# Optimization experiments

Hardware: AMD Instinct MI355X
Metric: run time of the kernel (lower is better)

Reference implementation:

```python
import jax, jax.numpy as jnp
import numpy as np

H = 64  # hidden size
T = 11  # unrolled timesteps


def setup_inputs() -> dict:
    key = jax.random.key(0)
    ks = jax.random.split(key, 8)
    B, V, E = 65536, 50000, 100
    return {
        "sent": jax.random.randint(ks[0], (B, T), 0, V, dtype=jnp.int32),
        "emb_W": jax.random.normal(ks[1], (V, E), jnp.float32) * 0.05,
        "W_ih": jax.random.normal(ks[2], (4 * H, E), jnp.float32) * 0.05,
        "W_hh": jax.random.normal(ks[3], (4 * H, H), jnp.float32) * 0.05,
        "b_ih": jax.random.normal(ks[4], (4 * H,), jnp.float32) * 0.05,
        "b_hh": jax.random.normal(ks[5], (4 * H,), jnp.float32) * 0.05,
        "fc_W": jax.random.normal(ks[6], (14, H), jnp.float32) * 0.05,
        "fc_b": jax.random.normal(ks[7], (14,), jnp.float32) * 0.05,
    }


def _lstm_cell(x, h, c, W_ih, W_hh, b_ih, b_hh):
    # gates order in torch LSTMCell: i, f, g, o
    gates = x @ W_ih.T + b_ih + h @ W_hh.T + b_hh  # [B, 4H]
    i, f, g, o = jnp.split(gates, 4, axis=-1)
    c_new = jax.nn.sigmoid(f) * c + jax.nn.sigmoid(i) * jnp.tanh(g)
    h_new = jax.nn.sigmoid(o) * jnp.tanh(c_new)
    return h_new, c_new


def reference(sent, emb_W, W_ih, W_hh, b_ih, b_hh, fc_W, fc_b):
    embed = emb_W[sent]  # [B, T, E]
    B = embed.shape[0]
    h0 = jnp.zeros((B, H), embed.dtype)
    c0 = jnp.zeros((B, H), embed.dtype)
    xs = jnp.swapaxes(embed[:, :T, :], 0, 1)  # [T, B, E]

    def step(carry, x):
        h, c = carry
        h, c = _lstm_cell(x, h, c, W_ih, W_hh, b_ih, b_hh)
        return (h, c), None

    (h_last, _), _ = jax.lax.scan(step, (h0, c0), xs)
    logits = h_last @ fc_W.T + fc_b  # [B, 14]
    return jax.nn.log_softmax(logits, axis=-1)
```

## Files before the change

kernel.cpp:

```cpp
#include <hip/hip_runtime.h>
#include <hip/hip_bf16.h>

#define T_STEPS 11
#define E_DIM   100
#define XSL     2048
#define NDMA    (2 * T_STEPS)

typedef int   i32x4   __attribute__((ext_vector_type(4)));
typedef float f32x4   __attribute__((ext_vector_type(4)));
typedef _Float16 h16x2 __attribute__((ext_vector_type(2)));
typedef _Float16 h16x4 __attribute__((ext_vector_type(4)));
typedef _Float16 h16x8 __attribute__((ext_vector_type(8)));

typedef __attribute__((address_space(1))) const unsigned int g_as1;
typedef __attribute__((address_space(3))) unsigned int l_as3;

__device__ __forceinline__ h16x2 spl2(float v) {
    _Float16 h = (_Float16)v;
    return (h16x2){h, h};
}
__device__ __forceinline__ h16x2 pk2(float a, float b) {
    return __builtin_bit_cast(h16x2, __builtin_amdgcn_cvt_pkrtz(a, b));
}
__device__ __forceinline__ unsigned char f2fp8(float f) {
    return (unsigned char)(__builtin_amdgcn_cvt_pk_fp8_f32(f, 0.f, 0, false) & 0xff);
}
__device__ __forceinline__ long long ll_lo(i32x4 v) {
    return ((long long)(unsigned)v[1] << 32) | (unsigned)v[0];
}
__device__ __forceinline__ long long ll_hi(i32x4 v) {
    return ((long long)(unsigned)v[3] << 32) | (unsigned)v[2];
}

__device__ __forceinline__ h16x2 tanh5(h16x2 x) {
    h16x2 x2 = x * x;
    h16x2 p = x2 * spl2(0.13333333f) + spl2(-0.33333333f);
    p = x2 * p + spl2(1.0f);
    return x * p;
}
__device__ __forceinline__ h16x2 tanh7(h16x2 x) {
    h16x2 x2 = x * x;
    h16x2 p = x2 * spl2(-0.05396825f) + spl2(0.13333333f);
    p = x2 * p + spl2(-0.33333333f);
    p = x2 * p + spl2(1.0f);
    return x * p;
}
__device__ __forceinline__ h16x2 sig3(h16x2 x) {
    h16x2 x2 = x * x;
    h16x2 p = x2 * spl2(-0.020833334f) + spl2(0.25f);
    return x * p + spl2(0.5f);
}

__global__ void pack_all(const float* __restrict__ emb,
                         const float* __restrict__ W_ih, const float* __restrict__ W_hh,
                         const float* __restrict__ b_ih, const float* __restrict__ b_hh,
                         unsigned char* __restrict__ embp8, unsigned char* __restrict__ Wx8,
                         unsigned char* __restrict__ Wh8, float* __restrict__ biasf, int V)
{
    int b = blockIdx.x;
    int tid = threadIdx.x;
    if (b < 128) {
        int id = b * 256 + tid;
        int n = id >> 7, k = id & 127;
        float v = (k < E_DIM) ? W_ih[n * E_DIM + k] : 0.f;
        int kt = k >> 5;
        int lane = (n & 15) | (((k & 31) >> 3) << 4);
        Wx8[((kt * 16 + (n >> 4)) * 64 + lane) * 8 + (k & 7)] = f2fp8(v);
    } else if (b < 192) {
        int id = (b - 128) * 256 + tid;
        int n = id >> 6, k = id & 63;
        int kt = k >> 5;
        int lane = (n & 15) | (((k & 31) >> 3) << 4);
        Wh8[((kt * 16 + (n >> 4)) * 64 + lane) * 8 + (k & 7)] = f2fp8(W_hh[n * 64 + k]);
    } else if (b == 192) {
        biasf[tid] = b_ih[tid] + b_hh[tid];
    } else {
        int id = (b - 193) * 256 + tid;
        if (id >= V * 8) return;
        int row = id >> 3;
        int c8 = id & 7;
        int p = c8 >> 2, qq = c8 & 3;
        const float* xr = emb + (size_t)row * E_DIM;
        float v[16];
        #pragma unroll
        for (int w = 0; w < 16; ++w) {
            int k = p * 64 + (w >> 3) * 32 + qq * 8 + (w & 7);
            v[w] = (k < E_DIM) ? xr[k] : 0.f;
        }
        int4 o;
        int* op = &o.x;
        #pragma unroll
        for (int w = 0; w < 4; ++w) {
            int d = __builtin_amdgcn_cvt_pk_fp8_f32(v[w*4+0], v[w*4+1], 0, false);
            d = __builtin_amdgcn_cvt_pk_fp8_f32(v[w*4+2], v[w*4+3], d, true);
            op[w] = d;
        }
        *reinterpret_cast<int4*>(embp8 + (size_t)row * 128 + c8 * 16) = o;
    }
}

template<int PACKED>
__global__ __launch_bounds__(256, 4)
void lstm_fused(const int* __restrict__ sent,
                const float* __restrict__ emb, const unsigned char* __restrict__ embp8,
                const unsigned char* __restrict__ Wx8, const unsigned char* __restrict__ Wh8,
                const float* __restrict__ biasf,
                const float* __restrict__ fc_W, const float* __restrict__ fc_b,
                float* __restrict__ out)
{
    __shared__ unsigned char xlds[T_STEPS * XSL];
    __shared__ unsigned char hlds[2][1024];
    __shared__ float biaslds[256];
    __shared__ short hscr[16 * 68];
    const int tid  = threadIdx.x;
    const int wv   = tid >> 6;
    const int lane = tid & 63;
    const int r    = lane & 15;
    const int q    = lane >> 4;
    const int b0   = blockIdx.x * 16;

    for (int d = wv; d < NDMA; d += 4) {
        int sl = d >> 1, half = d & 1;
        int c  = half * 4 + (lane >> 4);
        int rr = lane & 15;
        int idx = sent[(b0 + rr) * T_STEPS + sl];
        if (PACKED) {
            const unsigned char* src = embp8 + (size_t)idx * 128 + c * 16;
            __builtin_amdgcn_global_load_lds(
                (g_as1*)src, (l_as3*)&xlds[sl * XSL + half * 1024], 16, 0, 0);
        } else {
            const float* xr = emb + (size_t)idx * E_DIM;
            int p = c >> 2, qq = c & 3;
            float v[16];
            #pragma unroll
            for (int w = 0; w < 16; ++w) {
                int k = p * 64 + (w >> 3) * 32 + qq * 8 + (w & 7);
                v[w] = (k < E_DIM) ? xr[k] : 0.f;
            }
            int4 o;
            int* op = &o.x;
            #pragma unroll
            for (int w = 0; w < 4; ++w) {
                int dd = __builtin_amdgcn_cvt_pk_fp8_f32(v[w*4+0], v[w*4+1], 0, false);
                dd = __builtin_amdgcn_cvt_pk_fp8_f32(v[w*4+2], v[w*4+3], dd, true);
                op[w] = dd;
            }
            *reinterpret_cast<int4*>(&xlds[sl * XSL + (half * 64 + lane) * 16]) = o;
        }
    }

    long long wx[4][4], wh[2][4];
    #pragma unroll
    for (int kt = 0; kt < 4; ++kt)
        #pragma unroll
        for (int g = 0; g < 4; ++g)
            wx[kt][g] = *reinterpret_cast<const long long*>(
                Wx8 + ((kt * 16 + g * 4 + wv) * 64 + lane) * 8);
    #pragma unroll
    for (int kt = 0; kt < 2; ++kt)
        #pragma unroll
        for (int g = 0; g < 4; ++g)
            wh[kt][g] = *reinterpret_cast<const long long*>(
                Wh8 + ((kt * 16 + g * 4 + wv) * 64 + lane) * 8);
    #pragma unroll
    for (int kt = 0; kt < 4; ++kt)
        #pragma unroll
        for (int g = 0; g < 4; ++g)
            asm volatile("" : "+v"(wx[kt][g]));
    #pragma unroll
    for (int kt = 0; kt < 2; ++kt)
        #pragma unroll
        for (int g = 0; g < 4; ++g)
            asm volatile("" : "+v"(wh[kt][g]));

    biaslds[tid] = biasf[tid];
    reinterpret_cast<int*>(&hlds[0][0])[tid] = 0;

    __builtin_amdgcn_s_waitcnt(0);
    __syncthreads();

    auto acc_bias_x = [&](int sl, f32x4* acc) {
        #pragma unroll
        for (int g = 0; g < 4; ++g)
            acc[g] = *reinterpret_cast<const f32x4*>(
                &biaslds[(g * 4 + wv) * 16 + q * 4]);
        #pragma unroll
        for (int p = 0; p < 2; ++p) {
            i32x4 v = *reinterpret_cast<const i32x4*>(
                &xlds[sl * XSL + ((p * 4 + q) * 16 + r) * 16]);
            long long lo = ll_lo(v), hi = ll_hi(v);
            #pragma unroll
            for (int g = 0; g < 4; ++g)
                acc[g] = __builtin_amdgcn_mfma_f32_16x16x32_fp8_fp8(wx[2*p][g], lo, acc[g], 0, 0, 0);
            #pragma unroll
            for (int g = 0; g < 4; ++g)
                acc[g] = __builtin_amdgcn_mfma_f32_16x16x32_fp8_fp8(wx[2*p+1][g], hi, acc[g], 0, 0, 0);
        }
    };

    h16x2 c01 = spl2(0.f), c23 = spl2(0.f);
    f32x4 acc[4];
    acc_bias_x(0, acc);

    const int hq  = (wv & 1) * 2 + (q >> 1);
    const int hoff = (hq * 16 + r) * 16 + (wv >> 1) * 8 + (q & 1) * 4;

    #pragma unroll
    for (int t = 0; t < T_STEPS; ++t) {
        i32x4 hv = *reinterpret_cast<const i32x4*>(&hlds[t & 1][(q * 16 + r) * 16]);
        long long bh0 = ll_lo(hv), bh1 = ll_hi(hv);
        #pragma unroll
        for (int g = 0; g < 4; ++g)
            acc[g] = __builtin_amdgcn_mfma_f32_16x16x32_fp8_fp8(wh[0][g], bh0, acc[g], 0, 0, 0);
        #pragma unroll
        for (int g = 0; g < 4; ++g)
            acc[g] = __builtin_amdgcn_mfma_f32_16x16x32_fp8_fp8(wh[1][g], bh1, acc[g], 0, 0, 0);

        h16x2 gi0 = pk2(acc[0][0], acc[0][1]), gi1 = pk2(acc[0][2], acc[0][3]);
        h16x2 gf0 = pk2(acc[1][0], acc[1][1]), gf1 = pk2(acc[1][2], acc[1][3]);
        h16x2 gg0 = pk2(acc[2][0], acc[2][1]), gg1 = pk2(acc[2][2], acc[2][3]);
        h16x2 go0 = pk2(acc[3][0], acc[3][1]), go1 = pk2(acc[3][2], acc[3][3]);
        c01 = sig3(gf0) * c01 + sig3(gi0) * tanh5(gg0);
        c23 = sig3(gf1) * c23 + sig3(gi1) * tanh5(gg1);
        h16x2 h01 = sig3(go0) * tanh7(c01);
        h16x2 h23 = sig3(go1) * tanh7(c23);

        int hw = __builtin_amdgcn_cvt_pk_fp8_f32((float)h01[0], (float)h01[1], 0, false);
        hw = __builtin_amdgcn_cvt_pk_fp8_f32((float)h23[0], (float)h23[1], hw, true);
        *reinterpret_cast<int*>(&hlds[(t + 1) & 1][hoff]) = hw;

        if (t == T_STEPS - 1) {
            h16x4 hn = { h01[0], h01[1], h23[0], h23[1] };
            *reinterpret_cast<h16x4*>(&hscr[r * 68 + wv * 16 + q * 4]) = hn;
        }

        if (t + 1 < T_STEPS) acc_bias_x(t + 1, acc);

        __syncthreads();
    }

    const int row_local = wv * 4 + q;
    const int cls = r;
    const int brow = b0 + row_local;
    float s = (cls < 14) ? fc_b[cls] : 0.f;
    const float* wrow = fc_W + ((cls < 14) ? cls : 0) * 64;
    #pragma unroll
    for (int ch = 0; ch < 8; ++ch) {
        h16x8 hv8 = *reinterpret_cast<const h16x8*>(&hscr[row_local * 68 + ch * 8]);
        #pragma unroll
        for (int j = 0; j < 8; ++j)
            s = fmaf((float)hv8[j], wrow[ch * 8 + j], s);
    }
    float lg = (cls < 14) ? s : -1e30f;
    float mx = lg;
    mx = fmaxf(mx, __shfl_xor(mx, 1));
    mx = fmaxf(mx, __shfl_xor(mx, 2));
    mx = fmaxf(mx, __shfl_xor(mx, 4));
    mx = fmaxf(mx, __shfl_xor(mx, 8));
    float se = __expf(lg - mx);
    se += __shfl_xor(se, 1);
    se += __shfl_xor(se, 2);
    se += __shfl_xor(se, 4);
    se += __shfl_xor(se, 8);
    float lse = mx + __logf(se);
    if (cls < 14) out[(size_t)brow * 14 + cls] = lg - lse;
}

extern "C" void kernel_launch(void* const* d_in, const int* in_sizes, int n_in,
                              void* d_out, int out_size, void* d_ws, size_t ws_size,
                              hipStream_t stream)
{
    const int*   sent = (const int*)d_in[0];
    const float* emb  = (const float*)d_in[1];
    const float* W_ih = (const float*)d_in[2];
    const float* W_hh = (const float*)d_in[3];
    const float* b_ih = (const float*)d_in[4];
    const float* b_hh = (const float*)d_in[5];
    const float* fc_W = (const float*)d_in[6];
    const float* fc_b = (const float*)d_in[7];
    float* out = (float*)d_out;

    const int B = in_sizes[0] / T_STEPS;
    const int V = in_sizes[1] / E_DIM;
    const size_t emb_bytes = (size_t)V * 128;
    const size_t need = emb_bytes + 32768 + 16384 + 1024;
    const bool packed = ws_size >= need;

    unsigned char* embp8 = (unsigned char*)d_ws;
    unsigned char* Wx8   = embp8 + emb_bytes;
    unsigned char* Wh8   = Wx8 + 32768;
    float*         biasf = (float*)(Wh8 + 16384);
    if (!packed) {
        Wx8   = (unsigned char*)d_ws;
        Wh8   = Wx8 + 32768;
        biasf = (float*)(Wh8 + 16384);
        embp8 = nullptr;
    }

    const int grid = B / 16;
    if (packed) {
        int pgrid = 193 + (V * 8 + 255) / 256;
        pack_all<<<pgrid, 256, 0, stream>>>(emb, W_ih, W_hh, b_ih, b_hh,
                                            embp8, Wx8, Wh8, biasf, V);
        lstm_fused<1><<<grid, 256, 0, stream>>>(sent, emb, embp8, Wx8, Wh8,
                                                biasf, fc_W, fc_b, out);
    } else {
        pack_all<<<193, 256, 0, stream>>>(emb, W_ih, W_hh, b_ih, b_hh,
                                          nullptr, Wx8, Wh8, biasf, 0);
        lstm_fused<0><<<grid, 256, 0, stream>>>(sent, emb, nullptr, Wx8, Wh8,
                                                biasf, fc_W, fc_b, out);
    }
}
```

Baseline: 150.5 us.

## Gather fp32 embedding rows directly and drop the fp8 embedding pre-pack pass

```diff
diff --git a/kernel.cpp b/kernel.cpp
--- a/kernel.cpp
+++ b/kernel.cpp
@@ -4,7 +4,7 @@
 #define T_STEPS 11
 #define E_DIM   100
 #define XSL     2048
-#define NDMA    (2 * T_STEPS)
+#define NSTG    (2 * T_STEPS)
 
 typedef int   i32x4   __attribute__((ext_vector_type(4)));
 typedef float f32x4   __attribute__((ext_vector_type(4)));
@@ -12,9 +12,6 @@
 typedef _Float16 h16x4 __attribute__((ext_vector_type(4)));
 typedef _Float16 h16x8 __attribute__((ext_vector_type(8)));
 
-typedef __attribute__((address_space(1))) const unsigned int g_as1;
-typedef __attribute__((address_space(3))) unsigned int l_as3;
-
 __device__ __forceinline__ h16x2 spl2(float v) {
     _Float16 h = (_Float16)v;
     return (h16x2){h, h};
@@ -24,6 +21,10 @@
 }
 __device__ __forceinline__ unsigned char f2fp8(float f) {
     return (unsigned char)(__builtin_amdgcn_cvt_pk_fp8_f32(f, 0.f, 0, false) & 0xff);
+}
+__device__ __forceinline__ int pk8x4(f32x4 v) {
+    int d = __builtin_amdgcn_cvt_pk_fp8_f32(v[0], v[1], 0, false);
+    return __builtin_amdgcn_cvt_pk_fp8_f32(v[2], v[3], d, true);
 }
 __device__ __forceinline__ long long ll_lo(i32x4 v) {
     return ((long long)(unsigned)v[1] << 32) | (unsigned)v[0];
@@ -51,11 +52,10 @@
     return x * p + spl2(0.5f);
 }
 
-__global__ void pack_all(const float* __restrict__ emb,
-                         const float* __restrict__ W_ih, const float* __restrict__ W_hh,
+__global__ void pack_all(const float* __restrict__ W_ih, const float* __restrict__ W_hh,
                          const float* __restrict__ b_ih, const float* __restrict__ b_hh,
-                         unsigned char* __restrict__ embp8, unsigned char* __restrict__ Wx8,
-                         unsigned char* __restrict__ Wh8, float* __restrict__ biasf, int V)
+                         unsigned char* __restrict__ Wx8, unsigned char* __restrict__ Wh8,
+                         float* __restrict__ biasf)
 {
     int b = blockIdx.x;
     int tid = threadIdx.x;
@@ -72,37 +72,14 @@
         int kt = k >> 5;
         int lane = (n & 15) | (((k & 31) >> 3) << 4);
         Wh8[((kt * 16 + (n >> 4)) * 64 + lane) * 8 + (k & 7)] = f2fp8(W_hh[n * 64 + k]);
-    } else if (b == 192) {
+    } else {
         biasf[tid] = b_ih[tid] + b_hh[tid];
-    } else {
-        int id = (b - 193) * 256 + tid;
-        if (id >= V * 8) return;
-        int row = id >> 3;
-        int c8 = id & 7;
-        int p = c8 >> 2, qq = c8 & 3;
-        const float* xr = emb + (size_t)row * E_DIM;
-        float v[16];
-        #pragma unroll
-        for (int w = 0; w < 16; ++w) {
-            int k = p * 64 + (w >> 3) * 32 + qq * 8 + (w & 7);
-            v[w] = (k < E_DIM) ? xr[k] : 0.f;
-        }
-        int4 o;
-        int* op = &o.x;
-        #pragma unroll
-        for (int w = 0; w < 4; ++w) {
-            int d = __builtin_amdgcn_cvt_pk_fp8_f32(v[w*4+0], v[w*4+1], 0, false);
-            d = __builtin_amdgcn_cvt_pk_fp8_f32(v[w*4+2], v[w*4+3], d, true);
-            op[w] = d;
-        }
-        *reinterpret_cast<int4*>(embp8 + (size_t)row * 128 + c8 * 16) = o;
-    }
-}
-
-template<int PACKED>
+    }
+}
+
 __global__ __launch_bounds__(256, 4)
 void lstm_fused(const int* __restrict__ sent,
-                const float* __restrict__ emb, const unsigned char* __restrict__ embp8,
+                const float* __restrict__ emb,
                 const unsigned char* __restrict__ Wx8, const unsigned char* __restrict__ Wh8,
                 const float* __restrict__ biasf,
                 const float* __restrict__ fc_W, const float* __restrict__ fc_b,
@@ -119,34 +96,26 @@
     const int q    = lane >> 4;
     const int b0   = blockIdx.x * 16;
 
-    for (int d = wv; d < NDMA; d += 4) {
+    for (int d = wv; d < NSTG; d += 4) {
         int sl = d >> 1, half = d & 1;
         int c  = half * 4 + (lane >> 4);
         int rr = lane & 15;
         int idx = sent[(b0 + rr) * T_STEPS + sl];
-        if (PACKED) {
-            const unsigned char* src = embp8 + (size_t)idx * 128 + c * 16;
-            __builtin_amdgcn_global_load_lds(
-                (g_as1*)src, (l_as3*)&xlds[sl * XSL + half * 1024], 16, 0, 0);
-        } else {
-            const float* xr = emb + (size_t)idx * E_DIM;
-            int p = c >> 2, qq = c & 3;
-            float v[16];
-            #pragma unroll
-            for (int w = 0; w < 16; ++w) {
-                int k = p * 64 + (w >> 3) * 32 + qq * 8 + (w & 7);
-                v[w] = (k < E_DIM) ? xr[k] : 0.f;
-            }
-            int4 o;
-            int* op = &o.x;
-            #pragma unroll
-            for (int w = 0; w < 4; ++w) {
-                int dd = __builtin_amdgcn_cvt_pk_fp8_f32(v[w*4+0], v[w*4+1], 0, false);
-                dd = __builtin_amdgcn_cvt_pk_fp8_f32(v[w*4+2], v[w*4+3], dd, true);
-                op[w] = dd;
-            }
-            *reinterpret_cast<int4*>(&xlds[sl * XSL + (half * 64 + lane) * 16]) = o;
-        }
+        const float* xr = emb + (size_t)idx * E_DIM;
+        int p = c >> 2, qq = c & 3;
+        int k0 = p * 64 + qq * 8;
+        int kb = k0 + 32;
+        f32x4 a0 = *reinterpret_cast<const f32x4*>(xr + k0);
+        f32x4 a1 = *reinterpret_cast<const f32x4*>(xr + k0 + 4);
+        f32x4 bz = {0.f, 0.f, 0.f, 0.f};
+        f32x4 bb0 = (kb + 4 <= E_DIM) ? *reinterpret_cast<const f32x4*>(xr + kb) : bz;
+        f32x4 bb1 = (kb + 8 <= E_DIM) ? *reinterpret_cast<const f32x4*>(xr + kb + 4) : bz;
+        int4 o;
+        o.x = pk8x4(a0);
+        o.y = pk8x4(a1);
+        o.z = pk8x4(bb0);
+        o.w = pk8x4(bb1);
+        *reinterpret_cast<int4*>(&xlds[sl * XSL + (half * 64 + lane) * 16]) = o;
     }
 
     long long wx[4][4], wh[2][4];
@@ -176,7 +145,6 @@
     biaslds[tid] = biasf[tid];
     reinterpret_cast<int*>(&hlds[0][0])[tid] = 0;
 
-    __builtin_amdgcn_s_waitcnt(0);
     __syncthreads();
 
     auto acc_bias_x = [&](int sl, f32x4* acc) {
@@ -281,33 +249,14 @@
     float* out = (float*)d_out;
 
     const int B = in_sizes[0] / T_STEPS;
-    const int V = in_sizes[1] / E_DIM;
-    const size_t emb_bytes = (size_t)V * 128;
-    const size_t need = emb_bytes + 32768 + 16384 + 1024;
-    const bool packed = ws_size >= need;
-
-    unsigned char* embp8 = (unsigned char*)d_ws;
-    unsigned char* Wx8   = embp8 + emb_bytes;
+
+    unsigned char* Wx8   = (unsigned char*)d_ws;
     unsigned char* Wh8   = Wx8 + 32768;
     float*         biasf = (float*)(Wh8 + 16384);
-    if (!packed) {
-        Wx8   = (unsigned char*)d_ws;
-        Wh8   = Wx8 + 32768;
-        biasf = (float*)(Wh8 + 16384);
-        embp8 = nullptr;
-    }
+
+    pack_all<<<193, 256, 0, stream>>>(W_ih, W_hh, b_ih, b_hh, Wx8, Wh8, biasf);
 
     const int grid = B / 16;
-    if (packed) {
-        int pgrid = 193 + (V * 8 + 255) / 256;
-        pack_all<<<pgrid, 256, 0, stream>>>(emb, W_ih, W_hh, b_ih, b_hh,
-                                            embp8, Wx8, Wh8, biasf, V);
-        lstm_fused<1><<<grid, 256, 0, stream>>>(sent, emb, embp8, Wx8, Wh8,
-                                                biasf, fc_W, fc_b, out);
-    } else {
-        pack_all<<<193, 256, 0, stream>>>(emb, W_ih, W_hh, b_ih, b_hh,
-                                          nullptr, Wx8, Wh8, biasf, 0);
-        lstm_fused<0><<<grid, 256, 0, stream>>>(sent, emb, nullptr, Wx8, Wh8,
-                                                biasf, fc_W, fc_b, out);
-    }
-}
+    lstm_fused<<<grid, 256, 0, stream>>>(sent, emb, Wx8, Wh8, biasf,
+                                         fc_W, fc_b, out);
+}
```

After: 167.5 us. 1.11x slower.
